# Kernel tuning notes

Hardware: AMD Instinct MI355X
Metric: run time of the kernel (lower is better)

Reference implementation:

```python
import jax, jax.numpy as jnp
import numpy as np

NUM_NODES = 64
NUM_VISIBLE = 16
NUM_STEPS = 20
ENERGY_SCALE = 1.0


def setup_inputs() -> dict:
    key = jax.random.key(0)
    k1, k2, k3, k4 = jax.random.split(key, 4)
    B, E = 65536, 512
    embedding = jax.random.normal(k1, (B, E), dtype=jnp.float32)
    reward = jax.random.normal(k2, (B,), dtype=jnp.float32)
    pca_components = jax.random.normal(k3, (E, NUM_VISIBLE), dtype=jnp.float32)
    quadratic = jax.random.normal(k4, (NUM_NODES, NUM_NODES), dtype=jnp.float32) * 0.01
    return {"embedding": embedding, "reward": reward,
            "pca_components": pca_components, "quadratic": quadratic}


def reference(embedding, reward, pca_components, quadratic):
    B = embedding.shape[0]
    dtype = embedding.dtype

    # KPP fallback transform: PCA-style projection (B, E) @ (E, 16) -> (B, 16)
    rep = embedding @ pca_components
    visible_bias = rep[:, :NUM_VISIBLE]

    # per-sample linear bias, zeros except visible slots; BM bias = batch mean (no_grad)
    lb = jnp.zeros((B, NUM_NODES), dtype).at[:, :NUM_VISIBLE].set(visible_bias)
    b = jax.lax.stop_gradient(lb.mean(axis=0))  # (N,)

    # clamped visible state: sigmoid(2*r) broadcast to (B, NUM_VISIBLE)
    s_visible = jnp.broadcast_to(jax.nn.sigmoid(reward[:, None] * 2.0), (B, NUM_VISIBLE))

    Wsym = quadratic + quadratic.T  # symmetric coupling field

    key = jax.random.key(42)
    k_init, k_scan = jax.random.split(key)
    hidden0 = jax.random.bernoulli(k_init, 0.5, (B, NUM_NODES - NUM_VISIBLE)).astype(dtype)
    s0 = jnp.concatenate([s_visible, hidden0], axis=-1)  # (B, N)

    def gibbs_step(s, k):
        p = jax.nn.sigmoid(s @ Wsym + b)               # (B, N)
        s_new = jax.random.bernoulli(k, p).astype(dtype)
        s_new = s_new.at[:, :NUM_VISIBLE].set(s_visible)  # clamp visible units
        return s_new, None

    keys = jax.random.split(k_scan, NUM_STEPS)
    s_all, _ = jax.lax.scan(gibbs_step, s0, keys)

    # energy E(s) = -s^T Q s - b^T s  per sample
    energy = -jnp.einsum('bi,ij,bj->b', s_all, quadratic, s_all) - s_all @ b

    adjusted = reward - ENERGY_SCALE * energy
    return adjusted[:, None]  # (B, 1)
```

## Files before the change

kernel.cpp:

```cpp
#include <hip/hip_runtime.h>
#include <stdint.h>

#define NNODES 64
#define NVIS   16
#define NHID   48
#define NSTEPS 20
#define BATCH  65536
#define EDIM   512

typedef float f32x2 __attribute__((ext_vector_type(2)));
typedef float f32x4 __attribute__((ext_vector_type(4)));

__device__ __forceinline__ f32x2 pk_fma_lo(f32x2 s, f32x2 w, f32x2 c) {
  f32x2 d;
  asm("v_pk_fma_f32 %0, %1, %2, %3 op_sel:[0,0,0] op_sel_hi:[1,0,1]"
      : "=v"(d) : "v"(s), "v"(w), "v"(c));
  return d;
}
__device__ __forceinline__ f32x2 pk_fma_hi(f32x2 s, f32x2 w, f32x2 c) {
  f32x2 d;
  asm("v_pk_fma_f32 %0, %1, %2, %3 op_sel:[0,1,0] op_sel_hi:[1,1,1]"
      : "=v"(d) : "v"(s), "v"(w), "v"(c));
  return d;
}

__device__ __forceinline__ void tf2x32(uint32_t k0, uint32_t k1,
                                       uint32_t x0, uint32_t x1,
                                       uint32_t& o0, uint32_t& o1) {
  const uint32_t ks0 = k0, ks1 = k1, ks2 = k0 ^ k1 ^ 0x1BD11BDAu;
  x0 += ks0; x1 += ks1;
  const int rotA[4] = {13, 15, 26, 6};
  const int rotB[4] = {17, 29, 16, 24};
#pragma unroll
  for (int i = 0; i < 5; ++i) {
#pragma unroll
    for (int r = 0; r < 4; ++r) {
      const int rot = (i & 1) ? rotB[r] : rotA[r];
      x0 += x1;
      x1 = __builtin_rotateleft32(x1, rot);
      x1 ^= x0;
    }
    const uint32_t i0 = (i == 0 || i == 3) ? ks1 : (i == 1 || i == 4) ? ks2 : ks0;
    const uint32_t i1 = (i == 0 || i == 3) ? ks2 : (i == 1 || i == 4) ? ks0 : ks1;
    x0 += i0;
    x1 += i1 + (uint32_t)(i + 1);
  }
  o0 = x0; o1 = x1;
}

__device__ __forceinline__ uint32_t rbits32(uint32_t k0, uint32_t k1, uint32_t n) {
  uint32_t a, b;
  tf2x32(k0, k1, 0u, n, a, b);
  return a ^ b;
}

__device__ __forceinline__ float u01(uint32_t bits) {
  return __uint_as_float((bits >> 9) | 0x3f800000u) - 1.0f;
}

__device__ __forceinline__ f32x2 xla_expf2(f32x2 x) {
#pragma clang fp contract(off)
  f32x2 fx = __builtin_elementwise_floor(
      __builtin_elementwise_fma(x, (f32x2)1.44269504088896341f, (f32x2)0.5f));
  f32x2 tmp = 0.693359375f * fx;
  f32x2 z   = -2.12194440e-4f * fx;
  f32x2 xr  = x - tmp;
  xr = xr - z;
  f32x2 zz = xr * xr;
  f32x2 y = __builtin_elementwise_fma(xr, (f32x2)1.9875691500e-4f, (f32x2)1.3981999507e-3f);
  y = __builtin_elementwise_fma(y, xr, (f32x2)8.3334519073e-3f);
  y = __builtin_elementwise_fma(y, xr, (f32x2)4.1665795894e-2f);
  y = __builtin_elementwise_fma(y, xr, (f32x2)1.6666665459e-1f);
  y = __builtin_elementwise_fma(y, xr, (f32x2)5.0000001201e-1f);
  y = __builtin_elementwise_fma(y, zz, xr);
  y = y + 1.0f;
  int mx = (int)fx.x, my = (int)fx.y;
  f32x2 e;
  e.x = __int_as_float((mx + 127) << 23);
  e.y = __int_as_float((my + 127) << 23);
  f32x2 r; r.x = y.x * e.x; r.y = y.y * e.y;
  return r;
}

__device__ __forceinline__ f32x2 sigmoid2(f32x2 a) {
#pragma clang fp contract(off)
  f32x2 na; na.x = -a.x; na.y = -a.y;
  f32x2 e = xla_expf2(na);
  f32x2 r;
  r.x = 1.0f / (1.0f + e.x);
  r.y = 1.0f / (1.0f + e.y);
  return r;
}

__device__ __forceinline__ f32x2 dot_pk(const f32x4* __restrict__ swq,
                                        const f32x2* wp) {
  f32x2 acc = (f32x2)0.0f;
#pragma unroll
  for (int i = 0; i < 32; ++i) {
    f32x4 q = swq[i];
    f32x2 slo; slo.x = q.x; slo.y = q.y;
    f32x2 shi; shi.x = q.z; shi.y = q.w;
    acc = pk_fma_lo(slo, wp[i], acc);
    acc = pk_fma_hi(shi, wp[i], acc);
  }
  return acc;
}

__global__ __launch_bounds__(512) void colsum_kernel(const float4* __restrict__ emb4,
                                                     float4* __restrict__ partials4,
                                                     int nblk) {
  __shared__ float4 red[4][128];
  const int t = threadIdx.x;
  const int c4 = t & 127, rs = t >> 7;
  float4 acc = make_float4(0.f, 0.f, 0.f, 0.f);
  const int stride = nblk * 4;
  for (int r = blockIdx.x * 4 + rs; r < BATCH; r += stride) {
    float4 v = emb4[(size_t)r * 128 + c4];
    acc.x += v.x; acc.y += v.y; acc.z += v.z; acc.w += v.w;
  }
  red[rs][c4] = acc;
  __syncthreads();
  if (rs == 0) {
    float4 a = red[0][c4], b = red[1][c4], c = red[2][c4], d = red[3][c4];
    float4 s;
    s.x = (a.x + b.x) + (c.x + d.x);
    s.y = (a.y + b.y) + (c.y + d.y);
    s.z = (a.z + b.z) + (c.z + d.z);
    s.w = (a.w + b.w) + (c.w + d.w);
    partials4[(size_t)blockIdx.x * 128 + c4] = s;
  }
}

__global__ __launch_bounds__(512) void reduce_kernel(const float* __restrict__ partials,
                                                     float* __restrict__ level2, int per) {
  const int t = threadIdx.x;
  float a = 0.0f;
  const int s0 = blockIdx.x * per;
  for (int s = s0; s < s0 + per; ++s) a += partials[(size_t)s * EDIM + t];
  level2[(size_t)blockIdx.x * EDIM + t] = a;
}

__global__ __launch_bounds__(512) void prep_kernel(const float* __restrict__ pca,
                                                   const float* __restrict__ level2, int g2,
                                                   float* __restrict__ bvec,
                                                   unsigned* __restrict__ keys) {
  __shared__ float cs[EDIM];
  int t = threadIdx.x;
  float a = 0.0f;
  for (int i = 0; i < g2; ++i) a += level2[(size_t)i * EDIM + t];
  cs[t] = a;
  __syncthreads();
  if (t < NNODES) {
    float bj = 0.0f;
    if (t < NVIS) {
      for (int e = 0; e < EDIM; ++e) bj = fmaf(cs[e], pca[e * NVIS + t], bj);
      bj *= (1.0f / 65536.0f);
    }
    bvec[t] = bj;
  }
  if (t == 0) {
    uint32_t ki0, ki1, ks0, ks1;
    tf2x32(0u, 42u, 0u, 0u, ki0, ki1);
    tf2x32(0u, 42u, 0u, 1u, ks0, ks1);
    keys[0] = ki0; keys[1] = ki1;
    for (int s = 0; s < NSTEPS; ++s) {
      uint32_t y0, y1;
      tf2x32(ks0, ks1, 0u, (uint32_t)s, y0, y1);
      keys[2 + 2 * s] = y0;
      keys[3 + 2 * s] = y1;
    }
  }
}

__global__ __launch_bounds__(256) void gibbs_kernel(const float* __restrict__ reward,
                                                    const float* __restrict__ quadratic,
                                                    const float* __restrict__ bvec,
                                                    const unsigned* __restrict__ keys,
                                                    float* __restrict__ out) {
#pragma clang fp contract(off)
  __shared__ float Wl[NNODES][NNODES];
  __shared__ alignas(16) f32x2 sbuf[4][NNODES];

  const int tid = threadIdx.x;
  for (int i = tid; i < NNODES * NNODES; i += 256) {
    int k = i >> 6, j = i & 63;
    Wl[k][j] = quadratic[i] + quadratic[j * NNODES + k];
  }
  __syncthreads();

  const int wave = tid >> 6, lane = tid & 63;

  f32x2 wp[32];
#pragma unroll
  for (int i = 0; i < 32; ++i) {
    f32x2 w; w.x = Wl[2 * i][lane]; w.y = Wl[2 * i + 1][lane];
    wp[i] = w;
  }

  const int r0 = (blockIdx.x * 4 + wave) * 2, r1 = r0 + 1;
  const float rw0 = reward[r0], rw1 = reward[r1];
  f32x2 sv2 = sigmoid2((f32x2){rw0 * 2.0f, rw1 * 2.0f});

  const bool isvis = (lane < NVIS);
  const uint32_t n0 = (uint32_t)(r0 * NNODES + lane);
  const uint32_t n1 = (uint32_t)(r1 * NNODES + lane);

  f32x2 scur;
  {
    bool hb0 = false, hb1 = false;
    if (!isvis) {
      int jh = lane - NVIS;
      hb0 = (rbits32(keys[0], keys[1], (uint32_t)(r0 * NHID + jh)) >> 31) == 0u;
      hb1 = (rbits32(keys[0], keys[1], (uint32_t)(r1 * NHID + jh)) >> 31) == 0u;
    }
    scur.x = isvis ? sv2.x : (hb0 ? 1.0f : 0.0f);
    scur.y = isvis ? sv2.y : (hb1 ? 1.0f : 0.0f);
  }

  f32x2* sw = sbuf[wave];
  const f32x4* swq = (const f32x4*)sw;
  sw[lane] = scur;

  const uint2* kbuf = (const uint2*)(keys + 2);
  uint2 kk = kbuf[0];
#pragma unroll 1
  for (int t = 0; t < NSTEPS; ++t) {
    uint2 kn = kbuf[(t + 1 < NSTEPS) ? t + 1 : t];
    uint32_t b0 = rbits32(kk.x, kk.y, n0);
    uint32_t b1 = rbits32(kk.x, kk.y, n1);
    f32x2 u2; u2.x = u01(b0); u2.y = u01(b1);
    f32x2 a2 = dot_pk(swq, wp);
    f32x2 p2 = sigmoid2(a2);
    scur.x = isvis ? sv2.x : ((u2.x < p2.x) ? 1.0f : 0.0f);
    scur.y = isvis ? sv2.y : ((u2.y < p2.y) ? 1.0f : 0.0f);
    sw[lane] = scur;
    kk = kn;
  }

  f32x2 a2 = dot_pk(swq, wp);
  const float bj = bvec[lane];
  float c0 = scur.x * fmaf(0.5f, a2.x, bj);
  float c1 = scur.y * fmaf(0.5f, a2.y, bj);
#pragma unroll
  for (int off = 32; off; off >>= 1) {
    c0 += __shfl_xor(c0, off);
    c1 += __shfl_xor(c1, off);
  }
  if (lane == 0) {
    out[r0] = rw0 + c0;
    out[r1] = rw1 + c1;
  }
}

extern "C" void kernel_launch(void* const* d_in, const int* in_sizes, int n_in,
                              void* d_out, int out_size, void* d_ws, size_t ws_size,
                              hipStream_t stream) {
  const float* emb    = (const float*)d_in[0];
  const float* reward = (const float*)d_in[1];
  const float* pca    = (const float*)d_in[2];
  const float* quad   = (const float*)d_in[3];
  float* out = (float*)d_out;

  int nblk = 1024;
  while (nblk > 4 &&
         ws_size < (size_t)nblk * EDIM * 4 + (size_t)64 * EDIM * 4 + 4096)
    nblk >>= 1;
  const int g2  = (nblk >= 64) ? 64 : nblk;
  const int per = nblk / g2;

  float*    partials = (float*)d_ws;
  float*    level2   = partials + (size_t)nblk * EDIM;
  float*    bvec     = level2 + (size_t)64 * EDIM;
  unsigned* keys     = (unsigned*)(bvec + NNODES);

  colsum_kernel<<<nblk, 512, 0, stream>>>((const float4*)emb, (float4*)partials, nblk);
  reduce_kernel<<<g2, 512, 0, stream>>>(partials, level2, per);
  prep_kernel<<<1, 512, 0, stream>>>(pca, level2, g2, bvec, keys);
  gibbs_kernel<<<BATCH / 8, 256, 0, stream>>>(reward, quad, bvec, keys, out);
}
```

Measured before the change: 360.2 us.

## Precompute constant visible-unit contribution and pack sigmoid math into v_pk ops

The Gibbs kernel now computes the clamped visible units' 16-term contribution to the field once, before the loop, and the per-step dot product covers only the 48 hidden units. This cuts per-step FMAs and the weight registers held. The state buffer now reuses the Wl shared array after a barrier, and the sigmoid/exp polynomial uses packed v_pk_fma/mul/add instructions. An odd leftover duplicate sigmoid call on the negated reward is overwritten straight away and only adds a little redundant work.

```diff
diff --git a/kernel.cpp b/kernel.cpp
--- a/kernel.cpp
+++ b/kernel.cpp
@@ -21,6 +21,31 @@
   f32x2 d;
   asm("v_pk_fma_f32 %0, %1, %2, %3 op_sel:[0,1,0] op_sel_hi:[1,1,1]"
       : "=v"(d) : "v"(s), "v"(w), "v"(c));
+  return d;
+}
+__device__ __forceinline__ f32x2 pk_fma2(f32x2 a, f32x2 b, f32x2 c) {
+  f32x2 d;
+  asm("v_pk_fma_f32 %0, %1, %2, %3" : "=v"(d) : "v"(a), "v"(b), "v"(c));
+  return d;
+}
+__device__ __forceinline__ f32x2 pk_mul2(f32x2 a, f32x2 b) {
+  f32x2 d;
+  asm("v_pk_mul_f32 %0, %1, %2" : "=v"(d) : "v"(a), "v"(b));
+  return d;
+}
+__device__ __forceinline__ f32x2 pk_add2(f32x2 a, f32x2 b) {
+  f32x2 d;
+  asm("v_pk_add_f32 %0, %1, %2" : "=v"(d) : "v"(a), "v"(b));
+  return d;
+}
+__device__ __forceinline__ f32x2 pk_sub2(f32x2 a, f32x2 b) {
+  f32x2 d;
+  asm("v_pk_add_f32 %0, %1, %2 neg_lo:[0,1] neg_hi:[0,1]" : "=v"(d) : "v"(a), "v"(b));
+  return d;
+}
+__device__ __forceinline__ f32x2 pk_negsub2(f32x2 a, f32x2 b) {
+  f32x2 d;
+  asm("v_pk_add_f32 %0, %1, %2 neg_lo:[1,1] neg_hi:[1,1]" : "=v"(d) : "v"(a), "v"(b));
   return d;
 }
 
@@ -54,49 +79,48 @@
   return a ^ b;
 }
 
-__device__ __forceinline__ float u01(uint32_t bits) {
-  return __uint_as_float((bits >> 9) | 0x3f800000u) - 1.0f;
-}
-
-__device__ __forceinline__ f32x2 xla_expf2(f32x2 x) {
+__device__ __forceinline__ f32x2 sigmoid2_pk(f32x2 a) {
 #pragma clang fp contract(off)
-  f32x2 fx = __builtin_elementwise_floor(
-      __builtin_elementwise_fma(x, (f32x2)1.44269504088896341f, (f32x2)0.5f));
-  f32x2 tmp = 0.693359375f * fx;
-  f32x2 z   = -2.12194440e-4f * fx;
-  f32x2 xr  = x - tmp;
-  xr = xr - z;
-  f32x2 zz = xr * xr;
-  f32x2 y = __builtin_elementwise_fma(xr, (f32x2)1.9875691500e-4f, (f32x2)1.3981999507e-3f);
-  y = __builtin_elementwise_fma(y, xr, (f32x2)8.3334519073e-3f);
-  y = __builtin_elementwise_fma(y, xr, (f32x2)4.1665795894e-2f);
-  y = __builtin_elementwise_fma(y, xr, (f32x2)1.6666665459e-1f);
-  y = __builtin_elementwise_fma(y, xr, (f32x2)5.0000001201e-1f);
-  y = __builtin_elementwise_fma(y, zz, xr);
-  y = y + 1.0f;
+  const f32x2 cL2En  = (f32x2)(-1.44269504088896341f);
+  const f32x2 cHalf  = (f32x2)0.5f;
+  const f32x2 cLn2Hi = (f32x2)0.693359375f;
+  const f32x2 cLn2Lo = (f32x2)(-2.12194440e-4f);
+  const f32x2 c0 = (f32x2)1.9875691500e-4f, c1 = (f32x2)1.3981999507e-3f;
+  const f32x2 c2 = (f32x2)8.3334519073e-3f, c3 = (f32x2)4.1665795894e-2f;
+  const f32x2 c4 = (f32x2)1.6666665459e-1f, c5 = (f32x2)5.0000001201e-1f;
+  const f32x2 cOne = (f32x2)1.0f;
+
+  f32x2 t = pk_fma2(a, cL2En, cHalf);
+  f32x2 fx; fx.x = floorf(t.x); fx.y = floorf(t.y);
+  f32x2 tmp = pk_mul2(fx, cLn2Hi);
+  f32x2 z   = pk_mul2(fx, cLn2Lo);
+  f32x2 xr  = pk_negsub2(a, tmp);
+  xr = pk_sub2(xr, z);
+  f32x2 zz = pk_mul2(xr, xr);
+  f32x2 y = pk_fma2(xr, c0, c1);
+  y = pk_fma2(y, xr, c2);
+  y = pk_fma2(y, xr, c3);
+  y = pk_fma2(y, xr, c4);
+  y = pk_fma2(y, xr, c5);
+  y = pk_fma2(y, zz, xr);
+  y = pk_add2(y, cOne);
   int mx = (int)fx.x, my = (int)fx.y;
   f32x2 e;
   e.x = __int_as_float((mx + 127) << 23);
   e.y = __int_as_float((my + 127) << 23);
-  f32x2 r; r.x = y.x * e.x; r.y = y.y * e.y;
+  f32x2 ex = pk_mul2(y, e);
+  f32x2 den = pk_add2(ex, cOne);
+  f32x2 r;
+  r.x = 1.0f / den.x;
+  r.y = 1.0f / den.y;
   return r;
 }
 
-__device__ __forceinline__ f32x2 sigmoid2(f32x2 a) {
-#pragma clang fp contract(off)
-  f32x2 na; na.x = -a.x; na.y = -a.y;
-  f32x2 e = xla_expf2(na);
-  f32x2 r;
-  r.x = 1.0f / (1.0f + e.x);
-  r.y = 1.0f / (1.0f + e.y);
-  return r;
-}
-
-__device__ __forceinline__ f32x2 dot_pk(const f32x4* __restrict__ swq,
-                                        const f32x2* wp) {
-  f32x2 acc = (f32x2)0.0f;
-#pragma unroll
-  for (int i = 0; i < 32; ++i) {
+__device__ __forceinline__ f32x2 dot_hidden(const f32x4* __restrict__ swq,
+                                            const f32x2* wp, f32x2 acc16) {
+  f32x2 acc = acc16;
+#pragma unroll
+  for (int i = 0; i < 24; ++i) {
     f32x4 q = swq[i];
     f32x2 slo; slo.x = q.x; slo.y = q.y;
     f32x2 shi; shi.x = q.z; shi.y = q.w;
@@ -179,7 +203,6 @@
                                                     float* __restrict__ out) {
 #pragma clang fp contract(off)
   __shared__ float Wl[NNODES][NNODES];
-  __shared__ alignas(16) f32x2 sbuf[4][NNODES];
 
   const int tid = threadIdx.x;
   for (int i = tid; i < NNODES * NNODES; i += 256) {
@@ -190,55 +213,67 @@
 
   const int wave = tid >> 6, lane = tid & 63;
 
-  f32x2 wp[32];
-#pragma unroll
-  for (int i = 0; i < 32; ++i) {
-    f32x2 w; w.x = Wl[2 * i][lane]; w.y = Wl[2 * i + 1][lane];
-    wp[i] = w;
-  }
-
   const int r0 = (blockIdx.x * 4 + wave) * 2, r1 = r0 + 1;
   const float rw0 = reward[r0], rw1 = reward[r1];
-  f32x2 sv2 = sigmoid2((f32x2){rw0 * 2.0f, rw1 * 2.0f});
+  const float bj = bvec[lane];
+  f32x2 sv2 = sigmoid2_pk((f32x2){-rw0 * 2.0f, -rw1 * 2.0f});
+  sv2 = sigmoid2_pk((f32x2){rw0 * 2.0f, rw1 * 2.0f});
+
+  f32x2 wp[24];
+#pragma unroll
+  for (int i = 0; i < 24; ++i) {
+    f32x2 w; w.x = Wl[16 + 2 * i][lane]; w.y = Wl[17 + 2 * i][lane];
+    wp[i] = w;
+  }
+  f32x2 acc16 = (f32x2)0.0f;
+#pragma unroll
+  for (int i = 0; i < 8; ++i) {
+    f32x2 w; w.x = Wl[2 * i][lane]; w.y = Wl[2 * i + 1][lane];
+    acc16 = pk_fma_lo(sv2, w, acc16);
+    acc16 = pk_fma_hi(sv2, w, acc16);
+  }
+  __syncthreads();
+
+  f32x2* sw = ((f32x2*)&Wl[0][0]) + wave * NHID;
+  const f32x4* swq = (const f32x4*)sw;
 
   const bool isvis = (lane < NVIS);
   const uint32_t n0 = (uint32_t)(r0 * NNODES + lane);
   const uint32_t n1 = (uint32_t)(r1 * NNODES + lane);
 
-  f32x2 scur;
-  {
-    bool hb0 = false, hb1 = false;
-    if (!isvis) {
-      int jh = lane - NVIS;
-      hb0 = (rbits32(keys[0], keys[1], (uint32_t)(r0 * NHID + jh)) >> 31) == 0u;
-      hb1 = (rbits32(keys[0], keys[1], (uint32_t)(r1 * NHID + jh)) >> 31) == 0u;
-    }
-    scur.x = isvis ? sv2.x : (hb0 ? 1.0f : 0.0f);
-    scur.y = isvis ? sv2.y : (hb1 ? 1.0f : 0.0f);
-  }
-
-  f32x2* sw = sbuf[wave];
-  const f32x4* swq = (const f32x4*)sw;
-  sw[lane] = scur;
+  f32x2 scur = sv2;
+  if (!isvis) {
+    int jh = lane - NVIS;
+    bool hb0 = (rbits32(keys[0], keys[1], (uint32_t)(r0 * NHID + jh)) >> 31) == 0u;
+    bool hb1 = (rbits32(keys[0], keys[1], (uint32_t)(r1 * NHID + jh)) >> 31) == 0u;
+    scur.x = hb0 ? 1.0f : 0.0f;
+    scur.y = hb1 ? 1.0f : 0.0f;
+    sw[jh] = scur;
+  }
 
   const uint2* kbuf = (const uint2*)(keys + 2);
+  const f32x2 cOneU = (f32x2)1.0f;
   uint2 kk = kbuf[0];
 #pragma unroll 1
   for (int t = 0; t < NSTEPS; ++t) {
     uint2 kn = kbuf[(t + 1 < NSTEPS) ? t + 1 : t];
     uint32_t b0 = rbits32(kk.x, kk.y, n0);
     uint32_t b1 = rbits32(kk.x, kk.y, n1);
-    f32x2 u2; u2.x = u01(b0); u2.y = u01(b1);
-    f32x2 a2 = dot_pk(swq, wp);
-    f32x2 p2 = sigmoid2(a2);
-    scur.x = isvis ? sv2.x : ((u2.x < p2.x) ? 1.0f : 0.0f);
-    scur.y = isvis ? sv2.y : ((u2.y < p2.y) ? 1.0f : 0.0f);
-    sw[lane] = scur;
+    f32x2 um;
+    um.x = __uint_as_float((b0 >> 9) | 0x3f800000u);
+    um.y = __uint_as_float((b1 >> 9) | 0x3f800000u);
+    f32x2 u2 = pk_sub2(um, cOneU);
+    f32x2 a2 = dot_hidden(swq, wp, acc16);
+    f32x2 p2 = sigmoid2_pk(a2);
+    if (!isvis) {
+      scur.x = (u2.x < p2.x) ? 1.0f : 0.0f;
+      scur.y = (u2.y < p2.y) ? 1.0f : 0.0f;
+      sw[lane - NVIS] = scur;
+    }
     kk = kn;
   }
 
-  f32x2 a2 = dot_pk(swq, wp);
-  const float bj = bvec[lane];
+  f32x2 a2 = dot_hidden(swq, wp, acc16);
   float c0 = scur.x * fmaf(0.5f, a2.x, bj);
   float c1 = scur.y * fmaf(0.5f, a2.y, bj);
 #pragma unroll
```

Measured after the change: 330.2 us. -8.3%, faster.
